# Performance work log

Measured on AMD Instinct MI355X. Metric: run time of the kernel, lower is better.

## Reference

```python
import jax, jax.numpy as jnp
import numpy as np

# config constants (assumed; see notes)
OSC_COUPLING = 0.1
AMP_DECAY = 0.1
AMP_SAT = 1.0
HOPF_MU = 1.0
H = 1024
N_OSC = 64  # min(N_OSCILLATORS=64, H//8=128)


def leaky_relu(x, slope=0.2):
    return jnp.where(x >= 0, x, slope * x)


def setup_inputs() -> dict:
    key = jax.random.key(0)
    ks = jax.random.split(key, 16)
    B, S = 4, 2048
    sc_h = 1.0 / np.sqrt(H)
    sc_2n = 1.0 / np.sqrt(2 * N_OSC)
    return {
        "x": jax.random.normal(ks[0], (B, S, H), jnp.float32),
        "t": jax.random.uniform(ks[1], (B, S, 1), jnp.float32),
        # to_oscillator: Linear(H,H) -> LeakyReLU -> Linear(H, 2*N_OSC)
        "W1": jax.random.normal(ks[2], (H, H), jnp.float32) * sc_h,
        "b1": jnp.zeros((H,), jnp.float32),
        "W2": jax.random.normal(ks[3], (H, 2 * N_OSC), jnp.float32) * sc_h,
        "b2": jnp.zeros((2 * N_OSC,), jnp.float32),
        # from_oscillator: Linear(2*N_OSC,H) -> LeakyReLU -> Linear(H,H)
        "W3": jax.random.normal(ks[4], (2 * N_OSC, H), jnp.float32) * sc_2n,
        "b3": jnp.zeros((H,), jnp.float32),
        "W4": jax.random.normal(ks[5], (H, H), jnp.float32) * sc_h,
        "b4": jnp.zeros((H,), jnp.float32),
        # time_mod: Linear(1, N_OSC)
        "Wt": jax.random.normal(ks[6], (1, N_OSC), jnp.float32),
        "bt": jnp.zeros((N_OSC,), jnp.float32),
        "coupling": jax.random.normal(ks[7], (N_OSC, N_OSC), jnp.float32) * OSC_COUPLING,
        "frequencies": jnp.linspace(0.5, 2.0, N_OSC, dtype=jnp.float32),
        "mu": jnp.float32(HOPF_MU),
    }


def reference(x, t, W1, b1, W2, b2, W3, b3, W4, b4, Wt, bt, coupling, frequencies, mu):
    n = frequencies.shape[0]
    # to_oscillator MLP
    h = leaky_relu(x @ W1 + b1)
    osc = h @ W2 + b2                       # [B,S,2n]
    phase, amplitude = osc[..., :n], osc[..., n:]
    t_mod = t @ Wt + bt                      # [B,S,n]

    # NOTE: original loop reads phase[:, i-1] / amplitude[:, i-1] from the
    # ORIGINAL tensors, so steps are independent -> vectorize over time.
    pp = phase[:, :-1]                       # [B,S-1,n] prev phase
    diff = pp[..., :, None] - pp[..., None, :]   # [B,S-1,n,n]
    # sum over last dim of sin(diff) @ coupling == einsum with coupling row-sums
    csum = coupling.sum(axis=1)              # [n]
    coupling_sum = jnp.einsum('bsjm,m->bsj', jnp.sin(diff), csum)
    dphase = frequencies + coupling_sum * OSC_COUPLING + t_mod[:, 1:] * 0.1
    phase_new = pp + dphase * 0.1

    ap = amplitude[:, :-1]
    damp = (-AMP_DECAY + mu) * ap - ap ** 3
    amp_new = jnp.tanh(ap + damp * 0.1) * AMP_SAT

    phase_out = jnp.concatenate([phase[:, :1], phase_new], axis=1)
    amp_out = jnp.concatenate([amplitude[:, :1], amp_new], axis=1)
    combined = jnp.concatenate([phase_out, amp_out], axis=-1)  # [B,S,2n]

    # from_oscillator MLP
    h2 = leaky_relu(combined @ W3 + b3)
    oscillator_output = h2 @ W4 + b4
    return x + oscillator_output * 0.1
```

## Files before the change

kernel.cpp:

```cpp
#include <hip/hip_runtime.h>
#include <hip/hip_bf16.h>

typedef __hip_bfloat16 bf16;
typedef __attribute__((ext_vector_type(4))) float f32x4;
typedef __attribute__((ext_vector_type(8))) short short8;

#define BM 128
#define BN 128
#define BK 64

__device__ __forceinline__ void gload_lds16(const void* g, void* l) {
  __builtin_amdgcn_global_load_lds((const __attribute__((address_space(1))) void*)g,
                                   (__attribute__((address_space(3))) void*)l, 16, 0, 0);
}

template<int EPI>
__global__ __launch_bounds__(256)
void gemm_kernel(const bf16* __restrict__ A, const bf16* __restrict__ Bt,
                 const float* __restrict__ bias, const float* __restrict__ X,
                 void* __restrict__ Cout, int M, int N, int K)
{
  __shared__ bf16 As[BM * BK];
  __shared__ bf16 Bs[BN * BK];
  const int tid  = threadIdx.x;
  const int lane = tid & 63;
  const int wr   = (tid >> 6) >> 1;
  const int wc   = (tid >> 6) & 1;
  const long bm  = (long)blockIdx.x * BM;
  const long bn  = (long)blockIdx.y * BN;

  f32x4 acc[4][4] = {};

  int frow[4], fcol[4], fdst[4];
#pragma unroll
  for (int c = 0; c < 4; ++c) {
    int f    = (c * 256 + tid) * 16;
    int row  = f >> 7;
    int bcol = (f & 127) ^ ((row & 7) << 4);
    frow[c] = row;
    fcol[c] = bcol >> 1;
    fdst[c] = f;
  }

  const int nK = K / BK;
  for (int kt = 0; kt < nK; ++kt) {
    const int kb = kt * BK;
    __syncthreads();
#pragma unroll
    for (int c = 0; c < 4; ++c) {
      gload_lds16(A  + (bm + frow[c]) * (long)K + kb + fcol[c], (char*)As + fdst[c]);
      gload_lds16(Bt + (bn + frow[c]) * (long)K + kb + fcol[c], (char*)Bs + fdst[c]);
    }
    __syncthreads();

#pragma unroll
    for (int ks = 0; ks < 2; ++ks) {
      short8 af[4], bfr[4];
      const int kcolb = (ks * 32 + (lane >> 4) * 8) * 2;
#pragma unroll
      for (int m = 0; m < 4; ++m) {
        int rr = wr * 64 + m * 16 + (lane & 15);
        af[m] = *(const short8*)((const char*)As + rr * 128 + (kcolb ^ ((rr & 7) << 4)));
      }
#pragma unroll
      for (int n = 0; n < 4; ++n) {
        int rr = wc * 64 + n * 16 + (lane & 15);
        bfr[n] = *(const short8*)((const char*)Bs + rr * 128 + (kcolb ^ ((rr & 7) << 4)));
      }
#pragma unroll
      for (int m = 0; m < 4; ++m)
#pragma unroll
        for (int n = 0; n < 4; ++n)
          acc[m][n] = __builtin_amdgcn_mfma_f32_16x16x32_bf16(af[m], bfr[n], acc[m][n], 0, 0, 0);
    }
  }

#pragma unroll
  for (int n = 0; n < 4; ++n) {
    const long col = bn + wc * 64 + n * 16 + (lane & 15);
    const float bv = bias[col];
#pragma unroll
    for (int m = 0; m < 4; ++m) {
      const long row0 = bm + wr * 64 + m * 16 + ((lane >> 4) << 2);
#pragma unroll
      for (int q = 0; q < 4; ++q) {
        float v = acc[m][n][q] + bv;
        const long idx = (row0 + q) * (long)N + col;
        if (EPI == 0) {
          v = (v >= 0.f) ? v : 0.2f * v;
          ((bf16*)Cout)[idx] = __float2bfloat16(v);
        } else if (EPI == 1) {
          ((float*)Cout)[idx] = v;
        } else {
          ((float*)Cout)[idx] = X[idx] + 0.1f * v;
        }
      }
    }
  }
}

__global__ void convert_bf16_kernel(const float* __restrict__ in, bf16* __restrict__ out, int n4)
{
  int i = blockIdx.x * blockDim.x + threadIdx.x;
  const int stride = gridDim.x * blockDim.x;
  for (; i < n4; i += stride) {
    const float4 v = ((const float4*)in)[i];
    union { bf16 b[4]; uint2 u; } pk;
    pk.b[0] = __float2bfloat16(v.x); pk.b[1] = __float2bfloat16(v.y);
    pk.b[2] = __float2bfloat16(v.z); pk.b[3] = __float2bfloat16(v.w);
    ((uint2*)out)[i] = pk.u;
  }
}

__global__ void transpose_f32_bf16(const float* __restrict__ in, bf16* __restrict__ out,
                                   int R, int C)
{
  __shared__ float tile[32][33];
  const int bx = blockIdx.x * 32;
  const int by = blockIdx.y * 32;
  const int tx = threadIdx.x, ty = threadIdx.y;
#pragma unroll
  for (int i = ty; i < 32; i += 8)
    tile[i][tx] = in[(size_t)(by + i) * C + bx + tx];
  __syncthreads();
#pragma unroll
  for (int i = ty; i < 32; i += 8)
    out[(size_t)(bx + i) * R + by + tx] = __float2bfloat16(tile[tx][i]);
}

__global__ void csum_kernel(const float* __restrict__ coupling, float* __restrict__ csum)
{
  const int m = threadIdx.x;
  float s = 0.f;
#pragma unroll
  for (int n = 0; n < 64; ++n) s += coupling[m * 64 + n];
  csum[m] = s;
}

__global__ void middle_kernel(const float* __restrict__ osc, const float* __restrict__ t,
                              const float* __restrict__ Wt, const float* __restrict__ bt,
                              const float* __restrict__ freq, const float* __restrict__ csum,
                              const float* __restrict__ mu_p, bf16* __restrict__ combined,
                              int nrows, int S)
{
  const int r = blockIdx.x * 4 + (threadIdx.x >> 6);
  const int j = threadIdx.x & 63;
  if (r >= nrows) return;
  const int s = r & (S - 1);
  float ph, am;
  if (s == 0) {
    ph = osc[(size_t)r * 128 + j];
    am = osc[(size_t)r * 128 + 64 + j];
  } else {
    const float p = osc[(size_t)(r - 1) * 128 + j];
    const float a = osc[(size_t)(r - 1) * 128 + 64 + j];
    float sp, cp;
    sincosf(p, &sp, &cp);
    const float cw = csum[j];
    float sumc = cp * cw, sums = sp * cw;
#pragma unroll
    for (int off = 32; off; off >>= 1) {
      sumc += __shfl_xor(sumc, off);
      sums += __shfl_xor(sums, off);
    }
    const float coupling_sum = sp * sumc - cp * sums;
    const float tm = t[r] * Wt[j] + bt[j];
    const float dp = freq[j] + coupling_sum * 0.1f + tm * 0.1f;
    ph = p + dp * 0.1f;
    const float mu = mu_p[0];
    const float u = a + 0.1f * ((mu - 0.1f) * a - a * a * a);
    am = tanhf(u);
  }
  combined[(size_t)r * 128 + j]      = __float2bfloat16(ph);
  combined[(size_t)r * 128 + 64 + j] = __float2bfloat16(am);
}

extern "C" void kernel_launch(void* const* d_in, const int* in_sizes, int n_in,
                              void* d_out, int out_size, void* d_ws, size_t ws_size,
                              hipStream_t stream)
{
  const float* x        = (const float*)d_in[0];
  const float* t        = (const float*)d_in[1];
  const float* W1       = (const float*)d_in[2];
  const float* b1       = (const float*)d_in[3];
  const float* W2       = (const float*)d_in[4];
  const float* b2       = (const float*)d_in[5];
  const float* W3       = (const float*)d_in[6];
  const float* b3       = (const float*)d_in[7];
  const float* W4       = (const float*)d_in[8];
  const float* b4       = (const float*)d_in[9];
  const float* Wt       = (const float*)d_in[10];
  const float* bt       = (const float*)d_in[11];
  const float* coupling = (const float*)d_in[12];
  const float* freq     = (const float*)d_in[13];
  const float* mu       = (const float*)d_in[14];

  const int Mrows = 8192;
  const int S     = 2048;

  char* ws = (char*)d_ws;
  size_t o = 0;
  auto alloc = [&](size_t bytes) {
    char* p = ws + o;
    o = (o + bytes + 255) & ~(size_t)255;
    return p;
  };
  bf16* xw_h2    = (bf16*)alloc((size_t)Mrows * 1024 * 2);
  bf16* hbuf     = (bf16*)alloc((size_t)Mrows * 1024 * 2);
  bf16* W1t      = (bf16*)alloc((size_t)1024 * 1024 * 2);
  bf16* W4t      = (bf16*)alloc((size_t)1024 * 1024 * 2);
  bf16* W2t      = (bf16*)alloc((size_t)1024 * 128 * 2);
  bf16* W3t      = (bf16*)alloc((size_t)1024 * 128 * 2);
  float* osc     = (float*)alloc((size_t)Mrows * 128 * 4);
  bf16* combined = (bf16*)alloc((size_t)Mrows * 128 * 2);
  float* csum    = (float*)alloc(64 * 4);

  convert_bf16_kernel<<<2048, 256, 0, stream>>>(x, xw_h2, Mrows * 1024 / 4);
  transpose_f32_bf16<<<dim3(32, 32), dim3(32, 8), 0, stream>>>(W1, W1t, 1024, 1024);
  transpose_f32_bf16<<<dim3(4, 32),  dim3(32, 8), 0, stream>>>(W2, W2t, 1024, 128);
  transpose_f32_bf16<<<dim3(32, 4),  dim3(32, 8), 0, stream>>>(W3, W3t, 128, 1024);
  transpose_f32_bf16<<<dim3(32, 32), dim3(32, 8), 0, stream>>>(W4, W4t, 1024, 1024);
  csum_kernel<<<1, 64, 0, stream>>>(coupling, csum);

  gemm_kernel<0><<<dim3(64, 8), 256, 0, stream>>>(xw_h2, W1t, b1, nullptr, hbuf, Mrows, 1024, 1024);
  gemm_kernel<1><<<dim3(64, 1), 256, 0, stream>>>(hbuf, W2t, b2, nullptr, osc, Mrows, 128, 1024);
  middle_kernel<<<Mrows / 4, 256, 0, stream>>>(osc, t, Wt, bt, freq, csum, mu, combined, Mrows, S);
  gemm_kernel<0><<<dim3(64, 8), 256, 0, stream>>>(combined, W3t, b3, nullptr, xw_h2, Mrows, 1024, 128);
  gemm_kernel<2><<<dim3(64, 8), 256, 0, stream>>>(xw_h2, W4t, b4, x, d_out, Mrows, 1024, 1024);
}
```

Before: 210.3 us.

## Split-K the narrow W2 GEMM and swizzle block order for XCD locality

The narrow N=128 GEMM previously launched only 64 workgroups. It now splits K into four partitions along grid z, which writes four partial fp32 outputs, and the middle kernel sums them and adds the bias. The large GEMMs also remap block IDs so consecutive workgroups land on the same XCD group, aiming for better L2 reuse of A/B tiles. The cost is extra partial-buffer traffic and a larger workspace.

```diff
diff --git a/kernel.cpp b/kernel.cpp
--- a/kernel.cpp
+++ b/kernel.cpp
@@ -8,17 +8,19 @@
 #define BM 128
 #define BN 128
 #define BK 64
+#define MROWS 8192
+#define PARTSZ (MROWS * 128)
 
 __device__ __forceinline__ void gload_lds16(const void* g, void* l) {
   __builtin_amdgcn_global_load_lds((const __attribute__((address_space(1))) void*)g,
                                    (__attribute__((address_space(3))) void*)l, 16, 0, 0);
 }
 
-template<int EPI>
+template<int EPI, bool SWZ>
 __global__ __launch_bounds__(256)
 void gemm_kernel(const bf16* __restrict__ A, const bf16* __restrict__ Bt,
                  const float* __restrict__ bias, const float* __restrict__ X,
-                 void* __restrict__ Cout, int M, int N, int K)
+                 void* __restrict__ Cout, int M, int N, int K, int kLen)
 {
   __shared__ bf16 As[BM * BK];
   __shared__ bf16 Bs[BN * BK];
@@ -26,8 +28,22 @@
   const int lane = tid & 63;
   const int wr   = (tid >> 6) >> 1;
   const int wc   = (tid >> 6) & 1;
-  const long bm  = (long)blockIdx.x * BM;
-  const long bn  = (long)blockIdx.y * BN;
+
+  int bmI, bnI;
+  if (SWZ) {
+    const int nwg = gridDim.x * gridDim.y;
+    const int bid = blockIdx.x + gridDim.x * blockIdx.y;
+    const int cpx = nwg >> 3;
+    const int swz = (bid & 7) * cpx + (bid >> 3);
+    bmI = swz % gridDim.x;
+    bnI = swz / gridDim.x;
+  } else {
+    bmI = blockIdx.x;
+    bnI = blockIdx.y;
+  }
+  const long bm = (long)bmI * BM;
+  const long bn = (long)bnI * BN;
+  const int kOff = blockIdx.z * kLen;
 
   f32x4 acc[4][4] = {};
 
@@ -42,9 +58,9 @@
     fdst[c] = f;
   }
 
-  const int nK = K / BK;
+  const int nK = kLen / BK;
   for (int kt = 0; kt < nK; ++kt) {
-    const int kb = kt * BK;
+    const int kb = kOff + kt * BK;
     __syncthreads();
 #pragma unroll
     for (int c = 0; c < 4; ++c) {
@@ -75,10 +91,12 @@
     }
   }
 
+  char* Cbase = (char*)Cout;
+  if (EPI == 1) Cbase += (size_t)blockIdx.z * M * (size_t)N * 4;
 #pragma unroll
   for (int n = 0; n < 4; ++n) {
     const long col = bn + wc * 64 + n * 16 + (lane & 15);
-    const float bv = bias[col];
+    const float bv = (EPI == 1) ? 0.f : bias[col];
 #pragma unroll
     for (int m = 0; m < 4; ++m) {
       const long row0 = bm + wr * 64 + m * 16 + ((lane >> 4) << 2);
@@ -88,11 +106,11 @@
         const long idx = (row0 + q) * (long)N + col;
         if (EPI == 0) {
           v = (v >= 0.f) ? v : 0.2f * v;
-          ((bf16*)Cout)[idx] = __float2bfloat16(v);
+          ((bf16*)Cbase)[idx] = __float2bfloat16(v);
         } else if (EPI == 1) {
-          ((float*)Cout)[idx] = v;
+          ((float*)Cbase)[idx] = v;
         } else {
-          ((float*)Cout)[idx] = X[idx] + 0.1f * v;
+          ((float*)Cbase)[idx] = X[idx] + 0.1f * v;
         }
       }
     }
@@ -137,23 +155,30 @@
   csum[m] = s;
 }
 
-__global__ void middle_kernel(const float* __restrict__ osc, const float* __restrict__ t,
+__global__ void middle_kernel(const float* __restrict__ osc_part, const float* __restrict__ t,
                               const float* __restrict__ Wt, const float* __restrict__ bt,
                               const float* __restrict__ freq, const float* __restrict__ csum,
-                              const float* __restrict__ mu_p, bf16* __restrict__ combined,
-                              int nrows, int S)
+                              const float* __restrict__ mu_p, const float* __restrict__ b2,
+                              bf16* __restrict__ combined, int nrows, int S)
 {
   const int r = blockIdx.x * 4 + (threadIdx.x >> 6);
   const int j = threadIdx.x & 63;
   if (r >= nrows) return;
   const int s = r & (S - 1);
+  const int src = (s == 0) ? r : r - 1;
+  const size_t rs = (size_t)src * 128;
+
+  float p = b2[j], a = b2[64 + j];
+#pragma unroll
+  for (int kc = 0; kc < 4; ++kc) {
+    p += osc_part[(size_t)kc * PARTSZ + rs + j];
+    a += osc_part[(size_t)kc * PARTSZ + rs + 64 + j];
+  }
+
   float ph, am;
   if (s == 0) {
-    ph = osc[(size_t)r * 128 + j];
-    am = osc[(size_t)r * 128 + 64 + j];
+    ph = p; am = a;
   } else {
-    const float p = osc[(size_t)(r - 1) * 128 + j];
-    const float a = osc[(size_t)(r - 1) * 128 + 64 + j];
     float sp, cp;
     sincosf(p, &sp, &cp);
     const float cw = csum[j];
@@ -195,7 +220,7 @@
   const float* freq     = (const float*)d_in[13];
   const float* mu       = (const float*)d_in[14];
 
-  const int Mrows = 8192;
+  const int Mrows = MROWS;
   const int S     = 2048;
 
   char* ws = (char*)d_ws;
@@ -211,7 +236,7 @@
   bf16* W4t      = (bf16*)alloc((size_t)1024 * 1024 * 2);
   bf16* W2t      = (bf16*)alloc((size_t)1024 * 128 * 2);
   bf16* W3t      = (bf16*)alloc((size_t)1024 * 128 * 2);
-  float* osc     = (float*)alloc((size_t)Mrows * 128 * 4);
+  float* oscp    = (float*)alloc((size_t)4 * PARTSZ * 4);
   bf16* combined = (bf16*)alloc((size_t)Mrows * 128 * 2);
   float* csum    = (float*)alloc(64 * 4);
 
@@ -222,9 +247,14 @@
   transpose_f32_bf16<<<dim3(32, 32), dim3(32, 8), 0, stream>>>(W4, W4t, 1024, 1024);
   csum_kernel<<<1, 64, 0, stream>>>(coupling, csum);
 
-  gemm_kernel<0><<<dim3(64, 8), 256, 0, stream>>>(xw_h2, W1t, b1, nullptr, hbuf, Mrows, 1024, 1024);
-  gemm_kernel<1><<<dim3(64, 1), 256, 0, stream>>>(hbuf, W2t, b2, nullptr, osc, Mrows, 128, 1024);
-  middle_kernel<<<Mrows / 4, 256, 0, stream>>>(osc, t, Wt, bt, freq, csum, mu, combined, Mrows, S);
-  gemm_kernel<0><<<dim3(64, 8), 256, 0, stream>>>(combined, W3t, b3, nullptr, xw_h2, Mrows, 1024, 128);
-  gemm_kernel<2><<<dim3(64, 8), 256, 0, stream>>>(xw_h2, W4t, b4, x, d_out, Mrows, 1024, 1024);
-}
+  gemm_kernel<0, true><<<dim3(64, 8), 256, 0, stream>>>(xw_h2, W1t, b1, nullptr, hbuf,
+                                                        Mrows, 1024, 1024, 1024);
+  gemm_kernel<1, false><<<dim3(64, 1, 4), 256, 0, stream>>>(hbuf, W2t, nullptr, nullptr, oscp,
+                                                            Mrows, 128, 1024, 256);
+  middle_kernel<<<Mrows / 4, 256, 0, stream>>>(oscp, t, Wt, bt, freq, csum, mu, b2,
+                                               combined, Mrows, S);
+  gemm_kernel<0, true><<<dim3(64, 8), 256, 0, stream>>>(combined, W3t, b3, nullptr, xw_h2,
+                                                        Mrows, 1024, 128, 128);
+  gemm_kernel<2, true><<<dim3(64, 8), 256, 0, stream>>>(xw_h2, W4t, b4, x, d_out,
+                                                        Mrows, 1024, 1024, 1024);
+}
```

Result: no change. 208.9 us (-0.7%).
